# Performance work log

Measured on AMD Instinct MI355X. Metric: run time of the kernel, lower is better.

## Reference

```python
import jax, jax.numpy as jnp
import numpy as np
from jax import lax

NEIGHBORS = 3


def _dwconv(x, w, b, dil):
    # depthwise Conv3d, kernel (9,3,3), temporal pad 4, spatial dilation `dil`
    out = lax.conv_general_dilated(
        x, w, window_strides=(1, 1, 1),
        padding=[(4, 4), (dil, dil), (dil, dil)],
        rhs_dilation=(1, dil, dil),
        dimension_numbers=('NCDHW', 'OIDHW', 'NCDHW'),
        feature_group_count=w.shape[0])
    return out + b[None, :, None, None, None]


def setup_inputs() -> dict:
    key = jax.random.key(0)
    ks = jax.random.split(key, 20)
    N, C, T, H, W = 2, 512, 96, 14, 14
    rc = C // 16
    nrm = lambda k, shape: (jax.random.normal(k, shape, jnp.float32) * 0.02)
    inp = {
        'x': jax.random.normal(ks[0], (N, C, T, H, W), jnp.float32),
        'down_conv2_w': nrm(ks[1], (C, C)),
        'down_conv_w': nrm(ks[2], (rc, C)),
        'conv_back_w': nrm(ks[3], (C, rc)),
        'weights2': jnp.ones((2 * NEIGHBORS,), jnp.float32) / (2 * NEIGHBORS),
        'weights4': jnp.ones((3,), jnp.float32) / 3,
        'weights': jnp.ones((3,), jnp.float32) / 3,
        'query': jax.random.uniform(ks[4], (1, 1, C), jnp.float32),
        'q_w': nrm(ks[5], (C, C)), 'q_b': nrm(ks[6], (C,)),
        'k_w': nrm(ks[7], (C, C)), 'k_b': nrm(ks[8], (C,)),
        'v_w': nrm(ks[9], (C, C)), 'v_b': nrm(ks[10], (C,)),
        'c_w': nrm(ks[11], (C, C)), 'c_b': nrm(ks[12], (C,)),
        'sa1_w': nrm(ks[13], (rc, 1, 9, 3, 3)), 'sa1_b': nrm(ks[14], (rc,)),
        'sa2_w': nrm(ks[15], (rc, 1, 9, 3, 3)), 'sa2_b': nrm(ks[16], (rc,)),
        'sa3_w': nrm(ks[17], (rc, 1, 9, 3, 3)), 'sa3_b': nrm(ks[18], (rc,)),
    }
    return inp


def reference(x, down_conv2_w, down_conv_w, conv_back_w, weights2, weights4, weights,
              query, q_w, q_b, k_w, k_b, v_w, v_b, c_w, c_b,
              sa1_w, sa1_b, sa2_w, sa2_b, sa3_w, sa3_b):
    N, C, T, H, W = x.shape
    nb = NEIGHBORS
    win = 2 * nb + 1

    # --- AttentionPool2d: single head, single learned query token ---
    kv = x.reshape(N, C, T, H * W).transpose(3, 0, 2, 1).reshape(H * W, N * T, C)  # (L,B,C)
    q = jnp.broadcast_to(query, (1, N * T, C))
    qp = (q @ q_w.T + q_b) * (C ** -0.5)          # head_dim == C since num_heads=1
    kp = kv @ k_w.T + k_b
    vp = kv @ v_w.T + v_b
    attn = jax.nn.softmax(jnp.einsum('pbc,lbc->bpl', qp, kp), axis=-1)  # (B,1,L)
    att_out = jnp.einsum('bpl,lbc->pbc', attn, vp) @ c_w.T + c_b        # (1,B,C)
    x_att = att_out.reshape(1, N, T, C).transpose(1, 3, 2, 0)           # (N,C,T,1)

    # --- pooled queries ---
    x_mean = jnp.mean(x, axis=(3, 4))[..., None]   # (N,C,T,1)
    x_max = jnp.max(x, axis=(3, 4))[..., None]     # (N,C,T,1)
    xq = x_mean * weights4[0] + x_max * weights4[1] + x_att * weights4[2]

    # --- 1x1 conv + temporal unfold (window 7, zero pad 3), drop center frame ---
    x2 = jnp.einsum('oc,ncthw->nothw', down_conv2_w, x)
    xp = jnp.pad(x2, ((0, 0), (0, 0), (nb, nb), (0, 0), (0, 0)))
    windows = jnp.stack([xp[:, :, i:i + T] for i in range(win)], axis=3)  # (N,C,T,7,H,W)
    idx = np.array([i for i in range(win) if i != nb])                    # exclude center
    upfold = windows[:, :, :, idx] * weights2[None, None, None, :, None, None]
    upfold = upfold.reshape(N, C, T, 2 * nb * H * W)                      # (N,C,T,L)

    # --- local correlation / clustering with sigmoid-0.5 gating ---
    aff = jnp.einsum('nctp,nctl->ntpl', xq, upfold)                       # (N,T,1,L)
    feat = jnp.einsum('nctl,ntpl->nctp', upfold, jax.nn.sigmoid(aff) - 0.5)  # (N,C,T,1)
    features = feat[..., None]                                            # (N,C,T,1,1)

    # --- multi-branch dilated depthwise conv fusion ---
    x_down = jnp.einsum('oc,ncthw->nothw', down_conv_w, x)                # (N,rc,T,H,W)
    agg = (_dwconv(x_down, sa1_w, sa1_b, 1) * weights[0]
           + _dwconv(x_down, sa2_w, sa2_b, 2) * weights[1]
           + _dwconv(x_down, sa3_w, sa3_b, 3) * weights[2])
    agg = jnp.einsum('oc,ncthw->nothw', conv_back_w, agg)                 # (N,C,T,H,W)

    return features * (jax.nn.sigmoid(agg) - 0.5)
```

## Files before the change

kernel.cpp:

```cpp
#include <hip/hip_runtime.h>
#include <hip/hip_bf16.h>

using bf16 = __hip_bfloat16;
typedef __attribute__((ext_vector_type(4))) unsigned short ushort4v;

#define N_  2
#define C_  512
#define T_  96
#define H_  14
#define W_  14
#define HW_ 196
#define RC_ 32
#define B_  (N_*T_)
#define SC_ (T_*HW_)
#define XTOT (N_*C_*T_*HW_)

#define VQB   0
#define VKB   512
#define VVB   1024
#define VCB   1536
#define VQRY  2048
#define VSAB  2560
#define VW2   2688
#define VW4   2696
#define VWTS  2700
#define VECS_TOTAL 2720

__device__ __forceinline__ float b2f(bf16 v){ return __bfloat162float(v); }
__device__ __forceinline__ float u2f(unsigned short u){ return __uint_as_float(((unsigned)u)<<16); }
__device__ __forceinline__ float sigm(float x){ return 1.f/(1.f+__expf(-x)); }
__device__ __forceinline__ unsigned short f2bu(float f){
    bf16 b = __float2bfloat16(f);
    return *(unsigned short*)&b;
}

__device__ __forceinline__ float ldd(const void* p, size_t i, bool f32){
    if (f32) return ((const float*)p)[i];
    else     return b2f(((const bf16*)p)[i]);
}

__global__ void probe_kernel(const void* __restrict__ x, int* __restrict__ flag){
    if (blockIdx.x==0 && threadIdx.x==0){
        const unsigned short* h = (const unsigned short*)x;
        int wild = 0;
        for (int i=0;i<128;i++){
            int e = (h[i] >> 7) & 0xFF;
            if (e < 100 || e > 150) wild++;
        }
        flag[0] = (wild > 16) ? 1 : 0;
    }
}

__global__ void prep_w2t_kernel(const void* __restrict__ dcw2, float* __restrict__ w2t,
                                const int* __restrict__ flag){
    bool f32 = flag[0]!=0;
    int i = blockIdx.x*256 + threadIdx.x;
    if (i < C_*C_){
        int in = i / C_, out = i % C_;
        w2t[i] = ldd(dcw2, (size_t)out*C_ + in, f32);
    }
}

#define PM_OLD (16384+16384+7776+512*5+96+6+3+3)
#define PM_TOTAL (PM_OLD + 262144 + 262144)
__global__ void prep_misc_kernel(const void* dcw, const void* cbw,
                                 const void* sa1w, const void* sa2w, const void* sa3w,
                                 const void* q_b, const void* k_b, const void* v_b,
                                 const void* c_b, const void* query,
                                 const void* sa1b, const void* sa2b, const void* sa3b,
                                 const void* w2, const void* w4, const void* wts,
                                 const void* v_w, const void* c_w,
                                 float* __restrict__ dwt, float* __restrict__ cbwf,
                                 float* __restrict__ saw, float* __restrict__ vecs,
                                 float* __restrict__ vwt, float* __restrict__ cwt,
                                 const int* __restrict__ flag){
    bool f32 = flag[0]!=0;
    int i = blockIdx.x*256 + threadIdx.x;
    if (i >= PM_TOTAL) return;
    if (i < 16384){ int c=i>>5, r=i&31; dwt[i] = ldd(dcw, (size_t)r*C_+c, f32); return; }
    i -= 16384;
    if (i < 16384){ cbwf[i] = ldd(cbw, i, f32); return; }
    i -= 16384;
    if (i < 7776){
        const void* s = (i<2592)? sa1w : ((i<5184)? sa2w : sa3w);
        int j = (i<2592)? i : ((i<5184)? i-2592 : i-5184);
        saw[i] = ldd(s, j, f32); return;
    }
    i -= 7776;
    if (i < 512){ vecs[VQB +i] = ldd(q_b,  i, f32); return; } i -= 512;
    if (i < 512){ vecs[VKB +i] = ldd(k_b,  i, f32); return; } i -= 512;
    if (i < 512){ vecs[VVB +i] = ldd(v_b,  i, f32); return; } i -= 512;
    if (i < 512){ vecs[VCB +i] = ldd(c_b,  i, f32); return; } i -= 512;
    if (i < 512){ vecs[VQRY+i] = ldd(query,i, f32); return; } i -= 512;
    if (i < 96){
        const void* s = (i<32)? sa1b : ((i<64)? sa2b : sa3b);
        vecs[VSAB+i] = ldd(s, i&31, f32); return;
    }
    i -= 96;
    if (i < 6){ vecs[VW2+i] = ldd(w2, i, f32); return; } i -= 6;
    if (i < 3){ vecs[VW4+i] = ldd(w4, i, f32); return; } i -= 3;
    if (i < 3){ vecs[VWTS+i] = ldd(wts, i, f32); return; } i -= 3;
    if (i < 262144){ int r=i/C_, c=i%C_; vwt[i] = ldd(v_w, (size_t)c*C_+r, f32); return; }
    i -= 262144;
    { int r=i/C_, c=i%C_; cwt[i] = ldd(c_w, (size_t)c*C_+r, f32); }
}

#define TCH 128
__global__ void __launch_bounds__(256) cvt_tr_kernel(const void* __restrict__ x,
                                                     bf16* __restrict__ xt,
                                                     const int* __restrict__ flag){
    bool f32 = flag[0]!=0;
    int bt = blockIdx.x;
    int n = bt / T_, t = bt % T_;
    int c0 = blockIdx.y * TCH;
    __shared__ bf16 tile[TCH*197];
    int tid = threadIdx.x;
    const size_t ibase = (((size_t)n*C_ + c0)*T_ + t)*HW_;
    for (int i=tid; i<TCH*HW_; i+=256){
        int cr = i / HW_, l = i - cr*HW_;
        tile[cr*197 + l] = __float2bfloat16(ldd(x, ibase + (size_t)cr*SC_ + l, f32));
    }
    __syncthreads();
    bf16* obase = xt + (size_t)bt*HW_*C_ + c0;
    for (int i=tid; i<HW_*TCH; i+=256){
        int l = i >> 7, cl = i & 127;
        obase[(size_t)l*C_ + cl] = tile[cl*197 + l];
    }
}

__global__ void __launch_bounds__(64) qproj1_kernel(const void* __restrict__ q_w,
        const float* __restrict__ vecs, float* __restrict__ qp,
        const int* __restrict__ flag){
    bool f32 = flag[0]!=0;
    int c = blockIdx.x;
    int lane = threadIdx.x;
    float acc = 0.f;
    #pragma unroll
    for (int i=lane;i<C_;i+=64)
        acc += vecs[VQRY+i] * ldd(q_w, (size_t)c*C_+i, f32);
    #pragma unroll
    for (int off=32; off>0; off>>=1) acc += __shfl_down(acc, off);
    if (lane==0) qp[c] = (acc + vecs[VQB+c]) * 0.044194173824159216f;
}

__global__ void __launch_bounds__(256) qproj2_kernel(const void* __restrict__ k_w,
        const float* __restrict__ vecs, const float* __restrict__ qp,
        float* __restrict__ qk_out, const int* __restrict__ flag){
    bool f32 = flag[0]!=0;
    __shared__ float sh[256];
    int tid = threadIdx.x;
    if (blockIdx.x < 8){
        int c = blockIdx.x*64 + (tid&63);
        int isub = tid>>6;
        float acc = 0.f;
        for (int i=isub*128; i<isub*128+128; i++)
            acc += qp[i] * ldd(k_w, (size_t)i*C_ + c, f32);
        sh[tid] = acc;
        __syncthreads();
        if (tid < 64)
            qk_out[c] = sh[tid] + sh[tid+64] + sh[tid+128] + sh[tid+192];
    } else {
        float acc = 0.f;
        for (int i=tid;i<C_;i+=256) acc += qp[i]*vecs[VKB+i];
        sh[tid] = acc;
        __syncthreads();
        if (tid==0){
            float d=0.f;
            for (int i=0;i<256;i++) d += sh[i];
            qk_out[C_] = d;
        }
    }
}

__global__ void __launch_bounds__(512) f1_kernel(const bf16* __restrict__ xt,
        const float* __restrict__ qk, const float* __restrict__ vecs,
        float* __restrict__ pooled, float* __restrict__ mm){
    int b = blockIdx.x;
    __shared__ float sm[HW_];
    __shared__ float red[2];
    int tid = threadIdx.x, wave = tid>>6, lane = tid&63;
    float qkr[8];
    #pragma unroll
    for (int k=0;k<4;k++){ qkr[k] = qk[lane*4+k]; qkr[4+k] = qk[256+lane*4+k]; }
    float qkC = qk[C_];
    const bf16* fbase = xt + (size_t)b*HW_*C_;
    for (int l=wave; l<HW_; l+=8){
        const bf16* row = fbase + (size_t)l*C_;
        ushort4v u1 = *(const ushort4v*)(row + lane*4);
        ushort4v u2 = *(const ushort4v*)(row + 256 + lane*4);
        float a = 0.f;
        #pragma unroll
        for (int k=0;k<4;k++) a += qkr[k]*u2f(u1[k]) + qkr[4+k]*u2f(u2[k]);
        #pragma unroll
        for (int off=32; off>0; off>>=1) a += __shfl_down(a, off);
        if (lane==0) sm[l] = a + qkC;
    }
    __syncthreads();
    if (tid < 64){
        float m = -1e30f;
        for (int l=tid; l<HW_; l+=64) m = fmaxf(m, sm[l]);
        #pragma unroll
        for (int off=32; off>0; off>>=1) m = fmaxf(m, __shfl_down(m, off));
        if (tid==0) red[0] = m;
    }
    __syncthreads();
    if (tid < HW_) sm[tid] = __expf(sm[tid]-red[0]);
    __syncthreads();
    if (tid < 64){
        float s = 0.f;
        for (int l=tid; l<HW_; l+=64) s += sm[l];
        #pragma unroll
        for (int off=32; off>0; off>>=1) s += __shfl_down(s, off);
        if (tid==0) red[1] = 1.f/s;
    }
    __syncthreads();
    if (tid < HW_) sm[tid] *= red[1];
    __syncthreads();
    float w40=vecs[VW4+0], w41=vecs[VW4+1];
    int c = tid;
    const bf16* p = fbase + c;
    float s=0.f, m=-1e30f, pl=0.f;
    for (int l=0;l<HW_;l++){
        float v = u2f(*(const unsigned short*)(p + (size_t)l*C_));
        s += v; m = fmaxf(m, v); pl += sm[l]*v;
    }
    pooled[(size_t)b*C_+c] = pl;
    mm[(size_t)b*C_+c] = s*(1.f/HW_)*w40 + m*w41;
}

__global__ void __launch_bounds__(512) proj_kernel(const float* __restrict__ pooled,
        const float* __restrict__ mm, const float* __restrict__ vwt,
        const float* __restrict__ cwt, const void* __restrict__ dcw2,
        const float* __restrict__ vecs, float* __restrict__ xq,
        float* __restrict__ yq, const int* __restrict__ flag){
    bool f32 = flag[0]!=0;
    int b = blockIdx.x, c = threadIdx.x;
    __shared__ float p_s[C_];
    __shared__ float pre_s[C_];
    __shared__ float xq_s[C_];
    p_s[c] = pooled[(size_t)b*C_ + c];
    __syncthreads();
    float pre = vecs[VVB+c];
    for (int i=0;i<C_;i++) pre += p_s[i]*vwt[(size_t)i*C_+c];
    pre_s[c] = pre;
    __syncthreads();
    float att = vecs[VCB+c];
    for (int i=0;i<C_;i++) att += pre_s[i]*cwt[(size_t)i*C_+c];
    float xqv = mm[(size_t)b*C_+c] + vecs[VW4+2]*att;
    xq[(size_t)b*C_+c] = xqv;
    xq_s[c] = xqv;
    __syncthreads();
    float yqv = 0.f;
    for (int i=0;i<C_;i++) yqv += xq_s[i]*ldd(dcw2, (size_t)i*C_+c, f32);
    yq[(size_t)b*C_+c] = yqv;
}

__global__ void __launch_bounds__(256) corr2g_kernel(const bf16* __restrict__ xt,
        const float* __restrict__ yq, const float* __restrict__ vecs,
        float* __restrict__ g){
    const int offs[6] = {-3,-2,-1,1,2,3};
    int b = blockIdx.x, j = blockIdx.y;
    int n = b/T_, t = b%T_;
    int tj = t + offs[j];
    int tid = threadIdx.x, wave = tid>>6, lane = tid&63;
    if (tj < 0 || tj >= T_){
        if (tid < HW_) g[((size_t)b*6+j)*HW_ + tid] = 0.f;
        return;
    }
    float yqr[8];
    const float* yb = yq + (size_t)b*C_;
    #pragma unroll
    for (int k=0;k<4;k++){ yqr[k]=yb[lane*4+k]; yqr[4+k]=yb[256+lane*4+k]; }
    float w2j = vecs[VW2+j];
    const bf16* fbase = xt + ((size_t)n*T_ + tj)*HW_*C_;
    for (int l=wave; l<HW_; l+=4){
        const bf16* row = fbase + (size_t)l*C_;
        ushort4v u1 = *(const ushort4v*)(row + lane*4);
        ushort4v u2 = *(const ushort4v*)(row + 256 + lane*4);
        float a=0.f;
        #pragma unroll
        for (int k=0;k<4;k++) a += yqr[k]*u2f(u1[k]) + yqr[4+k]*u2f(u2[k]);
        #pragma unroll
        for (int off=32; off>0; off>>=1) a += __shfl_down(a, off);
        if (lane==0) g[((size_t)b*6+j)*HW_ + l] = w2j*(sigm(w2j*a)-0.5f);
    }
}

__global__ void __launch_bounds__(512) corr2z_kernel(const bf16* __restrict__ xt,
        const float* __restrict__ g, float* __restrict__ zbuf){
    const int offs[6] = {-3,-2,-1,1,2,3};
    int b = blockIdx.x, n=b/T_, t=b%T_;
    int tid = threadIdx.x;
    __shared__ float g_s[6*HW_];
    __shared__ float zred[4][C_];
    for (int i=tid;i<6*HW_;i+=512) g_s[i] = g[(size_t)b*6*HW_ + i];
    __syncthreads();
    int grp = tid>>7, te = tid&127;
    float a0=0.f,a1=0.f,a2=0.f,a3=0.f;
    #pragma unroll
    for (int j=0;j<6;j++){
        int tj = t+offs[j];
        if (tj<0||tj>=T_) continue;
        const bf16* fbase = xt + ((size_t)n*T_+tj)*HW_*C_ + te*4;
        const float* gj = g_s + j*HW_;
        for (int l=grp; l<HW_; l+=4){
            float gv = gj[l];
            ushort4v u = *(const ushort4v*)(fbase + (size_t)l*C_);
            a0 += gv*u2f(u[0]); a1 += gv*u2f(u[1]);
            a2 += gv*u2f(u[2]); a3 += gv*u2f(u[3]);
        }
    }
    zred[grp][te*4+0]=a0; zred[grp][te*4+1]=a1;
    zred[grp][te*4+2]=a2; zred[grp][te*4+3]=a3;
    __syncthreads();
    int e = tid;
    zbuf[(size_t)b*C_+e] = zred[0][e]+zred[1][e]+zred[2][e]+zred[3][e];
}

__global__ void __launch_bounds__(128) corr2f_kernel(const float* __restrict__ zbuf,
        const float* __restrict__ w2t, float* __restrict__ feat){
    int b = blockIdx.x, c0 = blockIdx.y*128;
    int tid = threadIdx.x;
    __shared__ float z_s[C_];
    for (int i=tid;i<C_;i+=128) z_s[i] = zbuf[(size_t)b*C_+i];
    __syncthreads();
    int c = c0 + tid;
    float acc = 0.f;
    for (int e=0;e<C_;e++) acc += w2t[(size_t)e*C_+c]*z_s[e];
    feat[(size_t)b*C_+c] = acc;
}

__global__ void __launch_bounds__(256) xdown_kernel(const bf16* __restrict__ xt,
                                                    const float* __restrict__ dwt,
                                                    bf16* __restrict__ xd){
    int b = blockIdx.x, n=b/T_, t=b%T_;
    int l0 = blockIdx.y*8;
    int nl = HW_ - l0; if (nl > 8) nl = 8;
    __shared__ bf16 xs[8*C_];
    int tid = threadIdx.x;
    const bf16* fbase = xt + (size_t)b*HW_*C_ + (size_t)l0*C_;
    for (int i=tid; i<nl*C_; i+=256) xs[i] = fbase[i];
    __syncthreads();
    int r = tid>>3, ls = tid&7;
    if (ls < nl){
        float acc = 0.f;
        for (int c=0;c<C_;c++)
            acc += dwt[c*RC_ + r] * b2f(xs[ls*C_ + c]);
        xd[(((size_t)n*RC_+r)*T_ + t)*HW_ + l0 + ls] = __float2bfloat16(acc);
    }
}

#define TPAD 21
#define TROW 20
#define TFRM (TROW*TPAD)
__global__ void __launch_bounds__(256) dwconv_kernel(const bf16* __restrict__ xd,
        const float* __restrict__ saw, const float* __restrict__ vecs,
        float* __restrict__ aggs){
    int nr = blockIdx.x;
    int t  = blockIdx.y;
    int r  = nr % RC_;
    __shared__ float tile[9*TFRM];
    __shared__ float wsm[3][81];
    int tid = threadIdx.x;
    for (int i=tid;i<9*TFRM;i+=256) tile[i] = 0.f;
    if (tid < 81){
        wsm[0][tid]=saw[       r*81+tid];
        wsm[1][tid]=saw[2592 + r*81+tid];
        wsm[2][tid]=saw[5184 + r*81+tid];
    }
    __syncthreads();
    const bf16* base = xd + (size_t)nr*T_*HW_;
    for (int i=tid;i<9*HW_;i+=256){
        int kt = i/HW_, hw = i - kt*HW_;
        int tg = t - 4 + kt;
        if (tg>=0 && tg<T_){
            int h = hw/W_, w = hw - h*W_;
            tile[kt*TFRM + (h+3)*TPAD + (w+3)] = b2f(base[(size_t)tg*HW_ + hw]);
        }
    }
    __syncthreads();
    if (tid < HW_){
        int h = tid/W_, w = tid - h*W_;
        float w0=vecs[VWTS+0], w1=vecs[VWTS+1], w2v=vecs[VWTS+2];
        float cbias = w0*vecs[VSAB+r] + w1*vecs[VSAB+32+r] + w2v*vecs[VSAB+64+r];
        float bacc[3];
        #pragma unroll
        for (int br=0;br<3;br++){
            int d = br+1;
            float s = 0.f;
            #pragma unroll
            for (int kt=0;kt<9;kt++){
                const float* tb = &tile[kt*TFRM + (h+3-d)*TPAD + (w+3-d)];
                const float* wp = &wsm[br][kt*9];
                s += wp[0]*tb[0]          + wp[1]*tb[d]          + wp[2]*tb[2*d]
                   + wp[3]*tb[d*TPAD]     + wp[4]*tb[d*TPAD+d]   + wp[5]*tb[d*TPAD+2*d]
                   + wp[6]*tb[2*d*TPAD]   + wp[7]*tb[2*d*TPAD+d] + wp[8]*tb[2*d*TPAD+2*d];
            }
            bacc[br] = s;
        }
        float acc = cbias + w0*bacc[0] + w1*bacc[1] + w2v*bacc[2];
        aggs[(size_t)nr*T_*HW_ + (size_t)t*HW_ + tid] = acc;
    }
}

__global__ void __launch_bounds__(256) final_kernel(const float* __restrict__ aggs,
                                                    const float* __restrict__ cbwf,
                                                    const float* __restrict__ feat,
                                                    float* __restrict__ out){
    int b = blockIdx.x, n = b/T_, t = b%T_;
    int c0 = blockIdx.y*128;
    int hw = threadIdx.x;
    if (hw >= HW_) return;
    float ra[RC_];
    #pragma unroll
    for (int r=0;r<RC_;r++)
        ra[r] = aggs[(((size_t)n*RC_+r)*T_ + t)*HW_ + hw];
    const float* fb = feat + (size_t)b*C_;
    for (int ci=0;ci<128;ci++){
        int c = c0+ci;
        const float* wr = cbwf + c*RC_;
        float a = 0.f;
        #pragma unroll
        for (int r=0;r<RC_;r++) a += wr[r]*ra[r];
        out[(((size_t)n*C_+c)*T_ + t)*HW_ + hw] = fb[c]*(sigm(a)-0.5f);
    }
}

extern "C" void kernel_launch(void* const* d_in, const int* in_sizes, int n_in,
                              void* d_out, int out_size, void* d_ws, size_t ws_size,
                              hipStream_t stream){
    const void* x      = d_in[0];
    const void* dcw2   = d_in[1];
    const void* dcw    = d_in[2];
    const void* cbw    = d_in[3];
    const void* w2     = d_in[4];
    const void* w4     = d_in[5];
    const void* wts    = d_in[6];
    const void* query  = d_in[7];
    const void* q_w    = d_in[8];
    const void* q_b    = d_in[9];
    const void* k_w    = d_in[10];
    const void* k_b    = d_in[11];
    const void* v_w    = d_in[12];
    const void* v_b    = d_in[13];
    const void* c_w    = d_in[14];
    const void* c_b    = d_in[15];
    const void* sa1w   = d_in[16];
    const void* sa1b   = d_in[17];
    const void* sa2w   = d_in[18];
    const void* sa2b   = d_in[19];
    const void* sa3w   = d_in[20];
    const void* sa3b   = d_in[21];
    float* out = (float*)d_out;

    float* ws    = (float*)d_ws;
    int*   flag  = (int*)ws;
    float* qk    = ws + 16;
    float* qp    = qk + 1024;
    float* pooled= qp + 1024;
    float* mm    = pooled + 98304;
    float* xq    = mm + 98304;
    float* yq    = xq + 98304;
    float* feat  = yq + 98304;
    float* w2t   = feat + 98304;
    float* vwt   = w2t + 262144;
    float* cwt   = vwt + 262144;
    float* dwt   = cwt + 262144;
    float* cbwf  = dwt + 16384;
    float* saw   = cbwf + 16384;
    float* vecs  = saw + 7936;
    float* aggs  = vecs + VECS_TOTAL;
    bf16*  xd    = (bf16*)(aggs + 1204224);
    float* g     = aggs;
    float* zbuf  = aggs + 225792;
    bf16*  xt    = (bf16*)d_out;

    probe_kernel<<<1, 64, 0, stream>>>(x, flag);
    prep_w2t_kernel<<<(C_*C_+255)/256, 256, 0, stream>>>(dcw2, w2t, flag);
    prep_misc_kernel<<<(PM_TOTAL+255)/256, 256, 0, stream>>>(
        dcw, cbw, sa1w, sa2w, sa3w, q_b, k_b, v_b, c_b, query,
        sa1b, sa2b, sa3b, w2, w4, wts, v_w, c_w,
        dwt, cbwf, saw, vecs, vwt, cwt, flag);
    cvt_tr_kernel<<<dim3(B_, C_/TCH), 256, 0, stream>>>(x, xt, flag);

    qproj1_kernel<<<C_, 64, 0, stream>>>(q_w, vecs, qp, flag);
    qproj2_kernel<<<9, 256, 0, stream>>>(k_w, vecs, qp, qk, flag);
    f1_kernel<<<B_, 512, 0, stream>>>(xt, qk, vecs, pooled, mm);
    proj_kernel<<<B_, C_, 0, stream>>>(pooled, mm, vwt, cwt, dcw2, vecs, xq, yq, flag);

    corr2g_kernel<<<dim3(B_, 6), 256, 0, stream>>>(xt, yq, vecs, g);
    corr2z_kernel<<<B_, 512, 0, stream>>>(xt, g, zbuf);
    corr2f_kernel<<<dim3(B_, 4), 128, 0, stream>>>(zbuf, w2t, feat);

    xdown_kernel<<<dim3(B_, 25), 256, 0, stream>>>(xt, dwt, xd);
    dwconv_kernel<<<dim3(N_*RC_, T_), 256, 0, stream>>>(xd, saw, vecs, aggs);
    final_kernel<<<dim3(B_, 4), 256, 0, stream>>>(aggs, cbwf, feat, out);
}
```

Measured before the change: 721.9 us.

## Fuse correlation gate and aggregation per source frame; vectorize f1 pooling loop

New measurement: 682.5 us. -5.5%, faster.

```diff
diff --git a/kernel.cpp b/kernel.cpp
--- a/kernel.cpp
+++ b/kernel.cpp
@@ -178,6 +178,7 @@
     int b = blockIdx.x;
     __shared__ float sm[HW_];
     __shared__ float red[2];
+    __shared__ float r8[8][C_];
     int tid = threadIdx.x, wave = tid>>6, lane = tid&63;
     float qkr[8];
     #pragma unroll
@@ -216,16 +217,46 @@
     __syncthreads();
     if (tid < HW_) sm[tid] *= red[1];
     __syncthreads();
+    float sa[8], pa[8], ma[8];
+    #pragma unroll
+    for (int k=0;k<8;k++){ sa[k]=0.f; pa[k]=0.f; ma[k]=-1e30f; }
+    for (int l=wave; l<HW_; l+=8){
+        const bf16* row = fbase + (size_t)l*C_;
+        ushort4v u1 = *(const ushort4v*)(row + lane*4);
+        ushort4v u2 = *(const ushort4v*)(row + 256 + lane*4);
+        float smv = sm[l];
+        #pragma unroll
+        for (int k=0;k<4;k++){
+            float v1 = u2f(u1[k]), v2 = u2f(u2[k]);
+            sa[k]   += v1; ma[k]   = fmaxf(ma[k],  v1); pa[k]   += smv*v1;
+            sa[4+k] += v2; ma[4+k] = fmaxf(ma[4+k],v2); pa[4+k] += smv*v2;
+        }
+    }
+    int c1 = lane*4, c2 = 256+lane*4;
+    #pragma unroll
+    for (int k=0;k<4;k++){ r8[wave][c1+k]=pa[k]; r8[wave][c2+k]=pa[4+k]; }
+    __syncthreads();
+    int c = tid;
+    float pltot = 0.f;
+    #pragma unroll
+    for (int w=0;w<8;w++) pltot += r8[w][c];
+    __syncthreads();
+    #pragma unroll
+    for (int k=0;k<4;k++){ r8[wave][c1+k]=sa[k]; r8[wave][c2+k]=sa[4+k]; }
+    __syncthreads();
+    float stot = 0.f;
+    #pragma unroll
+    for (int w=0;w<8;w++) stot += r8[w][c];
+    __syncthreads();
+    #pragma unroll
+    for (int k=0;k<4;k++){ r8[wave][c1+k]=ma[k]; r8[wave][c2+k]=ma[4+k]; }
+    __syncthreads();
+    float mtot = -1e30f;
+    #pragma unroll
+    for (int w=0;w<8;w++) mtot = fmaxf(mtot, r8[w][c]);
+    pooled[(size_t)b*C_+c] = pltot;
     float w40=vecs[VW4+0], w41=vecs[VW4+1];
-    int c = tid;
-    const bf16* p = fbase + c;
-    float s=0.f, m=-1e30f, pl=0.f;
-    for (int l=0;l<HW_;l++){
-        float v = u2f(*(const unsigned short*)(p + (size_t)l*C_));
-        s += v; m = fmaxf(m, v); pl += sm[l]*v;
-    }
-    pooled[(size_t)b*C_+c] = pl;
-    mm[(size_t)b*C_+c] = s*(1.f/HW_)*w40 + m*w41;
+    mm[(size_t)b*C_+c] = stot*(1.f/HW_)*w40 + mtot*w41;
 }
 
 __global__ void __launch_bounds__(512) proj_kernel(const float* __restrict__ pooled,
@@ -255,74 +286,98 @@
     yq[(size_t)b*C_+c] = yqv;
 }
 
-__global__ void __launch_bounds__(256) corr2g_kernel(const bf16* __restrict__ xt,
+#define QROWS 49
+#define B6C   (B_*6*C_)
+__global__ void __launch_bounds__(512) corr2gz_kernel(const bf16* __restrict__ xt,
         const float* __restrict__ yq, const float* __restrict__ vecs,
-        float* __restrict__ g){
+        float* __restrict__ zpart){
     const int offs[6] = {-3,-2,-1,1,2,3};
-    int b = blockIdx.x, j = blockIdx.y;
-    int n = b/T_, t = b%T_;
-    int tj = t + offs[j];
-    int tid = threadIdx.x, wave = tid>>6, lane = tid&63;
-    if (tj < 0 || tj >= T_){
-        if (tid < HW_) g[((size_t)b*6+j)*HW_ + tid] = 0.f;
-        return;
-    }
-    float yqr[8];
-    const float* yb = yq + (size_t)b*C_;
-    #pragma unroll
-    for (int k=0;k<4;k++){ yqr[k]=yb[lane*4+k]; yqr[4+k]=yb[256+lane*4+k]; }
-    float w2j = vecs[VW2+j];
-    const bf16* fbase = xt + ((size_t)n*T_ + tj)*HW_*C_;
-    for (int l=wave; l<HW_; l+=4){
-        const bf16* row = fbase + (size_t)l*C_;
-        ushort4v u1 = *(const ushort4v*)(row + lane*4);
-        ushort4v u2 = *(const ushort4v*)(row + 256 + lane*4);
-        float a=0.f;
-        #pragma unroll
-        for (int k=0;k<4;k++) a += yqr[k]*u2f(u1[k]) + yqr[4+k]*u2f(u2[k]);
-        #pragma unroll
-        for (int off=32; off>0; off>>=1) a += __shfl_down(a, off);
-        if (lane==0) g[((size_t)b*6+j)*HW_ + l] = w2j*(sigm(w2j*a)-0.5f);
-    }
-}
-
-__global__ void __launch_bounds__(512) corr2z_kernel(const bf16* __restrict__ xt,
-        const float* __restrict__ g, float* __restrict__ zbuf){
+    int frame = blockIdx.x;
+    int qq = blockIdx.y;
+    int n = frame / T_, tp = frame % T_;
+    int l0 = qq*QROWS;
+    __shared__ bf16 xs[QROWS*C_];
+    __shared__ float a_s[6][QROWS];
+    int tid = threadIdx.x, lane = tid&63, wave = tid>>6;
+    const ushort4v* src = (const ushort4v*)(xt + ((size_t)frame*HW_ + l0)*C_);
+    ushort4v* dst = (ushort4v*)xs;
+    for (int i=tid; i<QROWS*C_/4; i+=512) dst[i] = src[i];
+    bool val[6]; float w2r[6]; float yqr[6][8];
+    #pragma unroll
+    for (int jj=0;jj<6;jj++){
+        int tt = tp - offs[jj];
+        val[jj] = (tt>=0 && tt<T_);
+        w2r[jj] = vecs[VW2+jj];
+        if (val[jj]){
+            const float* yb = yq + (size_t)(n*T_+tt)*C_;
+            #pragma unroll
+            for (int k=0;k<4;k++){ yqr[jj][k]=yb[lane*4+k]; yqr[jj][4+k]=yb[256+lane*4+k]; }
+        } else {
+            #pragma unroll
+            for (int k=0;k<8;k++) yqr[jj][k]=0.f;
+        }
+    }
+    __syncthreads();
+    for (int li=wave; li<QROWS; li+=8){
+        ushort4v u1 = *(const ushort4v*)(xs + li*C_ + lane*4);
+        ushort4v u2 = *(const ushort4v*)(xs + li*C_ + 256 + lane*4);
+        float xf[8];
+        #pragma unroll
+        for (int k=0;k<4;k++){ xf[k]=u2f(u1[k]); xf[4+k]=u2f(u2[k]); }
+        float a[6];
+        #pragma unroll
+        for (int jj=0;jj<6;jj++){
+            float s=0.f;
+            #pragma unroll
+            for (int k=0;k<8;k++) s += yqr[jj][k]*xf[k];
+            a[jj]=s;
+        }
+        #pragma unroll
+        for (int off=32; off>0; off>>=1){
+            #pragma unroll
+            for (int jj=0;jj<6;jj++) a[jj] += __shfl_down(a[jj], off);
+        }
+        if (lane==0){
+            #pragma unroll
+            for (int jj=0;jj<6;jj++)
+                a_s[jj][li] = val[jj] ? w2r[jj]*(sigm(w2r[jj]*a[jj])-0.5f) : 0.f;
+        }
+    }
+    __syncthreads();
+    int e = tid;
+    float acc[6] = {0.f,0.f,0.f,0.f,0.f,0.f};
+    for (int li=0; li<QROWS; ++li){
+        float xv = b2f(xs[li*C_ + e]);
+        #pragma unroll
+        for (int jj=0;jj<6;jj++) acc[jj] += a_s[jj][li]*xv;
+    }
+    #pragma unroll
+    for (int jj=0;jj<6;jj++){
+        if (val[jj]){
+            int b = n*T_ + (tp - offs[jj]);
+            zpart[(size_t)qq*B6C + ((size_t)b*6+jj)*C_ + e] = acc[jj];
+        }
+    }
+}
+
+__global__ void __launch_bounds__(128) corr2f_kernel(const float* __restrict__ zpart,
+        const float* __restrict__ w2t, float* __restrict__ feat){
     const int offs[6] = {-3,-2,-1,1,2,3};
-    int b = blockIdx.x, n=b/T_, t=b%T_;
-    int tid = threadIdx.x;
-    __shared__ float g_s[6*HW_];
-    __shared__ float zred[4][C_];
-    for (int i=tid;i<6*HW_;i+=512) g_s[i] = g[(size_t)b*6*HW_ + i];
-    __syncthreads();
-    int grp = tid>>7, te = tid&127;
-    float a0=0.f,a1=0.f,a2=0.f,a3=0.f;
-    #pragma unroll
-    for (int j=0;j<6;j++){
-        int tj = t+offs[j];
-        if (tj<0||tj>=T_) continue;
-        const bf16* fbase = xt + ((size_t)n*T_+tj)*HW_*C_ + te*4;
-        const float* gj = g_s + j*HW_;
-        for (int l=grp; l<HW_; l+=4){
-            float gv = gj[l];
-            ushort4v u = *(const ushort4v*)(fbase + (size_t)l*C_);
-            a0 += gv*u2f(u[0]); a1 += gv*u2f(u[1]);
-            a2 += gv*u2f(u[2]); a3 += gv*u2f(u[3]);
-        }
-    }
-    zred[grp][te*4+0]=a0; zred[grp][te*4+1]=a1;
-    zred[grp][te*4+2]=a2; zred[grp][te*4+3]=a3;
-    __syncthreads();
-    int e = tid;
-    zbuf[(size_t)b*C_+e] = zred[0][e]+zred[1][e]+zred[2][e]+zred[3][e];
-}
-
-__global__ void __launch_bounds__(128) corr2f_kernel(const float* __restrict__ zbuf,
-        const float* __restrict__ w2t, float* __restrict__ feat){
     int b = blockIdx.x, c0 = blockIdx.y*128;
+    int t = b % T_;
     int tid = threadIdx.x;
     __shared__ float z_s[C_];
-    for (int i=tid;i<C_;i+=128) z_s[i] = zbuf[(size_t)b*C_+i];
+    for (int e=tid; e<C_; e+=128){
+        float s = 0.f;
+        #pragma unroll
+        for (int jj=0;jj<6;jj++){
+            int tj = t + offs[jj];
+            if (tj<0 || tj>=T_) continue;
+            const float* zp = zpart + ((size_t)b*6+jj)*C_ + e;
+            s += zp[0] + zp[B6C] + zp[2*B6C] + zp[3*(size_t)B6C];
+        }
+        z_s[e] = s;
+    }
     __syncthreads();
     int c = c0 + tid;
     float acc = 0.f;
@@ -471,9 +526,8 @@
     float* vecs  = saw + 7936;
     float* aggs  = vecs + VECS_TOTAL;
     bf16*  xd    = (bf16*)(aggs + 1204224);
-    float* g     = aggs;
-    float* zbuf  = aggs + 225792;
     bf16*  xt    = (bf16*)d_out;
+    float* zpart = (float*)(xt + (size_t)XTOT);
 
     probe_kernel<<<1, 64, 0, stream>>>(x, flag);
     prep_w2t_kernel<<<(C_*C_+255)/256, 256, 0, stream>>>(dcw2, w2t, flag);
@@ -488,9 +542,8 @@
     f1_kernel<<<B_, 512, 0, stream>>>(xt, qk, vecs, pooled, mm);
     proj_kernel<<<B_, C_, 0, stream>>>(pooled, mm, vwt, cwt, dcw2, vecs, xq, yq, flag);
 
-    corr2g_kernel<<<dim3(B_, 6), 256, 0, stream>>>(xt, yq, vecs, g);
-    corr2z_kernel<<<B_, 512, 0, stream>>>(xt, g, zbuf);
-    corr2f_kernel<<<dim3(B_, 4), 128, 0, stream>>>(zbuf, w2t, feat);
+    corr2gz_kernel<<<dim3(B_, 4), 512, 0, stream>>>(xt, yq, vecs, zpart);
+    corr2f_kernel<<<dim3(B_, 4), 128, 0, stream>>>(zpart, w2t, feat);
 
     xdown_kernel<<<dim3(B_, 25), 256, 0, stream>>>(xt, dwt, xd);
     dwconv_kernel<<<dim3(N_*RC_, T_), 256, 0, stream>>>(xd, saw, vecs, aggs);
```
